# Optimization experiments

Measured on AMD Instinct MI355X. Metric: run time of the kernel, lower is better.

The kernel has to match this reference:

```python
import jax, jax.numpy as jnp
import numpy as np

B = 2048        # number of independent sample paths (batched simulation)
DIM = 64        # SDE state dimension
NSTEPS = 500    # Euler steps: (t1-t0)/dt0 = 1.0/0.002
DT0 = 0.002


def setup_inputs() -> dict:
    key = jax.random.key(0)
    ks = jax.random.split(key, 6)
    s = 0.5 / np.sqrt(DIM)  # keep the linear SDE stable over the horizon
    return {
        "x0": jax.random.normal(ks[0], (B, DIM), jnp.float32),
        # raw N(0,1) noise; scaled by sqrt(dt) inside reference (Brownian increments)
        "dW": jax.random.normal(ks[1], (B, NSTEPS, DIM), jnp.float32),
        "drift": jax.random.normal(ks[2], (DIM, DIM), jnp.float32) * s,
        "drift_bias": jax.random.normal(ks[3], (DIM,), jnp.float32) * 0.1,
        "diffusion": jax.random.normal(ks[4], (DIM, DIM), jnp.float32) * (0.1 * s),
        "diffusion_bias": jax.random.normal(ks[5], (DIM,), jnp.float32) * 0.1,
        "ts": jnp.arange(NSTEPS + 1, dtype=jnp.float32) * DT0,
    }


def reference(x0, dW, drift, drift_bias, diffusion, diffusion_bias, ts):
    """Euler-Maruyama for dx = (A x + b) dt + diag(C x + d) dW.

    Matches the diffrax Euler solver with SaveAt(ts) where ts lies on the
    fixed-step grid. diag(C x + d) @ dW == (C x + d) * dW elementwise.
    Returns ys: [B, NSTEPS+1, DIM] (saved states at every ts, incl. x0).
    """
    dts = jnp.diff(ts)                       # [NSTEPS]
    dW_t = jnp.swapaxes(dW, 0, 1)            # [NSTEPS, B, DIM]

    def step(x, inp):
        dt, dw = inp
        drift_v = x @ drift.T + drift_bias                 # [B, DIM]
        diff_v = x @ diffusion.T + diffusion_bias          # [B, DIM]
        x_next = x + dt * drift_v + diff_v * (jnp.sqrt(dt) * dw)
        return x_next, x_next

    _, ys = jax.lax.scan(step, x0, (dts, dW_t))            # [NSTEPS, B, DIM]
    ys = jnp.concatenate([x0[None], ys], axis=0)           # [NSTEPS+1, B, DIM]
    return jnp.swapaxes(ys, 0, 1)                          # [B, NSTEPS+1, DIM]
```

## Files before the change

### kernel.cpp

```cpp
#include <hip/hip_runtime.h>

#define NPATH  2048
#define DIM    64
#define NSTEPS 500
#define PPW    16

typedef __attribute__((ext_vector_type(8))) short bf16x8;
typedef __attribute__((ext_vector_type(4))) float f32x4;

union FragU { bf16x8 v; unsigned int u[4]; uint4 q; };

__device__ __forceinline__ unsigned int pk_bf16(float lo, float hi) {
    unsigned int r;
    asm("v_cvt_pk_bf16_f32 %0, %1, %2" : "=v"(r) : "v"(lo), "v"(hi));
    return r;
}

#define MFMA __builtin_amdgcn_mfma_f32_16x16x32_bf16

__global__ __launch_bounds__(256, 1) void sde_mfma_mw2_kernel(
    const float* __restrict__ x0,
    const float* __restrict__ dW,
    const float* __restrict__ drift,
    const float* __restrict__ drift_bias,
    const float* __restrict__ diffusion,
    const float* __restrict__ diffusion_bias,
    const float* __restrict__ ts,
    float* __restrict__ out)
{
    __shared__ __align__(16) unsigned short xt[2][PPW * DIM];
    __shared__ float2 dtp[NSTEPS + 1];

    const int tid   = threadIdx.x;
    const int wn    = tid >> 6;
    const int lane  = tid & 63;
    const int c     = lane & 15;
    const int h     = lane >> 4;
    const int pbase = blockIdx.x * PPW;
    const int mydim = 16 * wn + c;

    for (int i = tid; i < NSTEPS; i += 256) {
        const float d = ts[i + 1] - ts[i];
        dtp[i] = make_float2(d, sqrtf(d));
    }
    if (tid == 0) dtp[NSTEPS] = make_float2(0.f, 0.f);

    FragU bd0, bd1, bs0, bs1;
    {
        const float* Ar = drift     + mydim * DIM + 8 * h;
        const float* Cr = diffusion + mydim * DIM + 8 * h;
        float4 t;
        t = *(const float4*)(Ar +  0); bd0.u[0] = pk_bf16(t.x, t.y); bd0.u[1] = pk_bf16(t.z, t.w);
        t = *(const float4*)(Ar +  4); bd0.u[2] = pk_bf16(t.x, t.y); bd0.u[3] = pk_bf16(t.z, t.w);
        t = *(const float4*)(Ar + 32); bd1.u[0] = pk_bf16(t.x, t.y); bd1.u[1] = pk_bf16(t.z, t.w);
        t = *(const float4*)(Ar + 36); bd1.u[2] = pk_bf16(t.x, t.y); bd1.u[3] = pk_bf16(t.z, t.w);
        t = *(const float4*)(Cr +  0); bs0.u[0] = pk_bf16(t.x, t.y); bs0.u[1] = pk_bf16(t.z, t.w);
        t = *(const float4*)(Cr +  4); bs0.u[2] = pk_bf16(t.x, t.y); bs0.u[3] = pk_bf16(t.z, t.w);
        t = *(const float4*)(Cr + 32); bs1.u[0] = pk_bf16(t.x, t.y); bs1.u[1] = pk_bf16(t.z, t.w);
        t = *(const float4*)(Cr + 36); bs1.u[2] = pk_bf16(t.x, t.y); bs1.u[3] = pk_bf16(t.z, t.w);
    }
    const float bdr = drift_bias[mydim];
    const float bdi = diffusion_bias[mydim];
    const f32x4 cbA = {bdr, bdr, bdr, bdr};
    const f32x4 cbC = {bdi, bdi, bdi, bdi};
    const f32x4 cz  = {0.f, 0.f, 0.f, 0.f};

    float xst[4];
    const float* dwq[4];
    float* op[4];
    unsigned int woff[4];
#pragma unroll
    for (int j = 0; j < 4; ++j) {
        const int pp = 4 * h + j;
        const int p  = pbase + pp;
        dwq[j] = dW  + (size_t)p * NSTEPS * DIM + mydim;
        op[j]  = out + (size_t)p * (NSTEPS + 1) * DIM + mydim;
        woff[j] = (unsigned)((pp * 32 + ((mydim >> 1) ^ ((pp & 7) << 2))) * 2 + (c & 1));
        const float v = x0[p * DIM + mydim];
        xst[j] = v;
        __builtin_nontemporal_store(v, op[j]);
        op[j] += DIM;
        xt[0][woff[j]] = (unsigned short)pk_bf16(v, v);
    }

    const int ra0 = c * 8 + (h ^ (c & 7));
    const int ra1 = c * 8 + ((4 + h) ^ (c & 7));
    const uint4* xr0 = (const uint4*)xt[0];
    const uint4* xr1 = (const uint4*)xt[1];
    unsigned short* xw0 = xt[0];
    unsigned short* xw1 = xt[1];

    float R0[4], R1[4], R2[4], R3[4], R4[4], R5[4], R6[4], R7[4];
#pragma unroll
    for (int j = 0; j < 4; ++j) {
        R0[j] = dwq[j][0 * DIM]; R1[j] = dwq[j][1 * DIM];
        R2[j] = dwq[j][2 * DIM]; R3[j] = dwq[j][3 * DIM];
        R4[j] = dwq[j][4 * DIM]; R5[j] = dwq[j][5 * DIM];
        R6[j] = dwq[j][6 * DIM]; R7[j] = dwq[j][7 * DIM];
        dwq[j] += 8 * DIM;
    }

    __syncthreads();

    float2 dts = dtp[0];

#define STEP(S, R, PF, KOFF, XR, XW)                                          \
    {                                                                         \
        FragU a0, a1;                                                         \
        a0.q = XR[ra0];                                                       \
        a1.q = XR[ra1];                                                       \
        const float srw0 = dts.y * R[0];   \
        const float srw1 = dts.y * R[1];                                      \
        const float srw2 = dts.y * R[2];                                      \
        const float srw3 = dts.y * R[3];                                      \
        if (PF) {                                                             \
            R[0] = dwq[0][(KOFF) * DIM];                                      \
            R[1] = dwq[1][(KOFF) * DIM];                                      \
            R[2] = dwq[2][(KOFF) * DIM];                                      \
            R[3] = dwq[3][(KOFF) * DIM];                                      \
        }                                                                     \
        const float2 dtn = dtp[(S) + 1];                                      \
        const f32x4 adA = MFMA(a0.v, bd0.v, cbA, 0, 0, 0);                    \
        const f32x4 adB = MFMA(a1.v, bd1.v, cz,  0, 0, 0);                    \
        const f32x4 ciA = MFMA(a0.v, bs0.v, cbC, 0, 0, 0);                    \
        const f32x4 ciB = MFMA(a1.v, bs1.v, cz,  0, 0, 0);                    \
        const float srw[4] = {srw0, srw1, srw2, srw3};                        \
        _Pragma("unroll")                                                     \
        for (int j = 0; j < 4; ++j) {                                         \
            const float ad = adA[j] + adB[j];                                 \
            const float ci = ciA[j] + ciB[j];                                 \
            const float xn = fmaf(dts.x, ad, xst[j]) + ci * srw[j];           \
            xst[j] = xn;                                                      \
            __builtin_nontemporal_store(xn, op[j]);                           \
            op[j] += DIM;                                                     \
            XW[woff[j]] = (unsigned short)pk_bf16(xn, xn);                    \
        }                                                                     \
        dts = dtn;                                                            \
        asm volatile("s_waitcnt lgkmcnt(0)" ::: "memory");                    \
        __builtin_amdgcn_s_barrier();                                         \
        __builtin_amdgcn_sched_barrier(0);                                    \
    }

    for (int it = 0; it < 61; ++it) {
        const int s = it * 8;
        STEP(s + 0, R0, 1, 0, xr0, xw1)
        STEP(s + 1, R1, 1, 1, xr1, xw0)
        STEP(s + 2, R2, 1, 2, xr0, xw1)
        STEP(s + 3, R3, 1, 3, xr1, xw0)
        STEP(s + 4, R4, 1, 4, xr0, xw1)
        STEP(s + 5, R5, 1, 5, xr1, xw0)
        STEP(s + 6, R6, 1, 6, xr0, xw1)
        STEP(s + 7, R7, 1, 7, xr1, xw0)
#pragma unroll
        for (int j = 0; j < 4; ++j) dwq[j] += 8 * DIM;
    }
    {
        STEP(488, R0, 1, 0, xr0, xw1)
        STEP(489, R1, 1, 1, xr1, xw0)
        STEP(490, R2, 1, 2, xr0, xw1)
        STEP(491, R3, 1, 3, xr1, xw0)
        STEP(492, R4, 0, 0, xr0, xw1)
        STEP(493, R5, 0, 0, xr1, xw0)
        STEP(494, R6, 0, 0, xr0, xw1)
        STEP(495, R7, 0, 0, xr1, xw0)
    }
    {
        STEP(496, R0, 0, 0, xr0, xw1)
        STEP(497, R1, 0, 0, xr1, xw0)
        STEP(498, R2, 0, 0, xr0, xw1)
        STEP(499, R3, 0, 0, xr1, xw0)
    }
#undef STEP
}

extern "C" void kernel_launch(void* const* d_in, const int* in_sizes, int n_in,
                              void* d_out, int out_size, void* d_ws, size_t ws_size,
                              hipStream_t stream) {
    const float* x0             = (const float*)d_in[0];
    const float* dW             = (const float*)d_in[1];
    const float* drift          = (const float*)d_in[2];
    const float* drift_bias     = (const float*)d_in[3];
    const float* diffusion      = (const float*)d_in[4];
    const float* diffusion_bias = (const float*)d_in[5];
    const float* ts             = (const float*)d_in[6];
    float* out = (float*)d_out;

    dim3 grid(NPATH / PPW);
    dim3 block(256);
    hipLaunchKernelGGL(sde_mfma_mw2_kernel, grid, block, 0, stream,
                       x0, dW, drift, drift_bias, diffusion, diffusion_bias,
                       ts, out);
}
```

Before: 138.2 us.

## Stream dW noise through an 8-slot LDS ring via global_load_lds DMA

Replaces per-thread register prefetch of the Brownian increments with direct global-to-LDS 16-byte DMA loads into a per-wave 8-deep ring buffer, gated by vmcnt waits, and reads the noise back from LDS each step. This aims to cut VGPR pressure and the number of scalar global loads, and to keep loads in flight across several steps. It also changes the output stores from nontemporal to normal stores. The vmcnt(16) accounting now mixes DMA loads with output stores, which adds risk of too much or too little waiting, and each step pays extra LDS reads.

Measured after the change: 400.7 us. +189.9%, slower.

```diff
diff --git a/kernel.cpp b/kernel.cpp
--- a/kernel.cpp
+++ b/kernel.cpp
@@ -16,9 +16,15 @@
     return r;
 }
 
+__device__ __forceinline__ void dma16(const float* src, float* lds) {
+    __builtin_amdgcn_global_load_lds(
+        (const __attribute__((address_space(1))) void*)src,
+        (__attribute__((address_space(3))) void*)lds, 16, 0, 0);
+}
+
 #define MFMA __builtin_amdgcn_mfma_f32_16x16x32_bf16
 
-__global__ __launch_bounds__(256, 1) void sde_mfma_mw2_kernel(
+__global__ __launch_bounds__(256, 1) void sde_mfma_dma_kernel(
     const float* __restrict__ x0,
     const float* __restrict__ dW,
     const float* __restrict__ drift,
@@ -29,6 +35,7 @@
     float* __restrict__ out)
 {
     __shared__ __align__(16) unsigned short xt[2][PPW * DIM];
+    __shared__ __align__(16) float ring[4][8][256];
     __shared__ float2 dtp[NSTEPS + 1];
 
     const int tid   = threadIdx.x;
@@ -66,19 +73,17 @@
     const f32x4 cz  = {0.f, 0.f, 0.f, 0.f};
 
     float xst[4];
-    const float* dwq[4];
     float* op[4];
     unsigned int woff[4];
 #pragma unroll
     for (int j = 0; j < 4; ++j) {
         const int pp = 4 * h + j;
         const int p  = pbase + pp;
-        dwq[j] = dW  + (size_t)p * NSTEPS * DIM + mydim;
         op[j]  = out + (size_t)p * (NSTEPS + 1) * DIM + mydim;
         woff[j] = (unsigned)((pp * 32 + ((mydim >> 1) ^ ((pp & 7) << 2))) * 2 + (c & 1));
         const float v = x0[p * DIM + mydim];
         xst[j] = v;
-        __builtin_nontemporal_store(v, op[j]);
+        *op[j] = v;
         op[j] += DIM;
         xt[0][woff[j]] = (unsigned short)pk_bf16(v, v);
     }
@@ -90,41 +95,42 @@
     unsigned short* xw0 = xt[0];
     unsigned short* xw1 = xt[1];
 
-    float R0[4], R1[4], R2[4], R3[4], R4[4], R5[4], R6[4], R7[4];
+    const float* pdma = dW + (size_t)(pbase + (lane >> 2)) * NSTEPS * DIM
+                           + 16 * wn + 4 * (lane & 3);
+    float (*ringw)[256] = ring[wn];
+    const int rbase = h * 64 + c;
+
 #pragma unroll
-    for (int j = 0; j < 4; ++j) {
-        R0[j] = dwq[j][0 * DIM]; R1[j] = dwq[j][1 * DIM];
-        R2[j] = dwq[j][2 * DIM]; R3[j] = dwq[j][3 * DIM];
-        R4[j] = dwq[j][4 * DIM]; R5[j] = dwq[j][5 * DIM];
-        R6[j] = dwq[j][6 * DIM]; R7[j] = dwq[j][7 * DIM];
-        dwq[j] += 8 * DIM;
-    }
+    for (int s = 0; s < 7; ++s)
+        dma16(pdma + (size_t)s * DIM, &ringw[s][0]);
+    pdma += 7 * DIM;
 
+    asm volatile("s_waitcnt vmcnt(0)" ::: "memory");
+    __builtin_amdgcn_sched_barrier(0);
     __syncthreads();
 
     float2 dts = dtp[0];
+    const float2* pdt = &dtp[1];
 
-#define STEP(S, R, PF, KOFF, XR, XW)                                          \
+#define STEP(K, DODMA, XR, XW)                                                \
     {                                                                         \
+        asm volatile("s_waitcnt vmcnt(16)" ::: "memory");                     \
+        __builtin_amdgcn_sched_barrier(0);                                    \
         FragU a0, a1;                                                         \
         a0.q = XR[ra0];                                                       \
         a1.q = XR[ra1];                                                       \
-        const float srw0 = dts.y * R[0];   \
-        const float srw1 = dts.y * R[1];                                      \
-        const float srw2 = dts.y * R[2];                                      \
-        const float srw3 = dts.y * R[3];                                      \
-        if (PF) {                                                             \
-            R[0] = dwq[0][(KOFF) * DIM];                                      \
-            R[1] = dwq[1][(KOFF) * DIM];                                      \
-            R[2] = dwq[2][(KOFF) * DIM];                                      \
-            R[3] = dwq[3][(KOFF) * DIM];                                      \
-        }                                                                     \
-        const float2 dtn = dtp[(S) + 1];                                      \
+        const float r0 = ringw[K][rbase +  0];                                \
+        const float r1 = ringw[K][rbase + 16];                                \
+        const float r2 = ringw[K][rbase + 32];                                \
+        const float r3 = ringw[K][rbase + 48];                                \
+        if (DODMA) dma16(pdma, &ringw[(K + 7) & 7][0]);                       \
+        pdma += DIM;                                                          \
+        const float2 dtn = *pdt++;                                            \
         const f32x4 adA = MFMA(a0.v, bd0.v, cbA, 0, 0, 0);                    \
         const f32x4 adB = MFMA(a1.v, bd1.v, cz,  0, 0, 0);                    \
         const f32x4 ciA = MFMA(a0.v, bs0.v, cbC, 0, 0, 0);                    \
         const f32x4 ciB = MFMA(a1.v, bs1.v, cz,  0, 0, 0);                    \
-        const float srw[4] = {srw0, srw1, srw2, srw3};                        \
+        const float srw[4] = {dts.y * r0, dts.y * r1, dts.y * r2, dts.y * r3};\
         _Pragma("unroll")                                                     \
         for (int j = 0; j < 4; ++j) {                                         \
             const float ad = adA[j] + adB[j];                                 \
@@ -142,34 +148,27 @@
     }
 
     for (int it = 0; it < 61; ++it) {
-        const int s = it * 8;
-        STEP(s + 0, R0, 1, 0, xr0, xw1)
-        STEP(s + 1, R1, 1, 1, xr1, xw0)
-        STEP(s + 2, R2, 1, 2, xr0, xw1)
-        STEP(s + 3, R3, 1, 3, xr1, xw0)
-        STEP(s + 4, R4, 1, 4, xr0, xw1)
-        STEP(s + 5, R5, 1, 5, xr1, xw0)
-        STEP(s + 6, R6, 1, 6, xr0, xw1)
-        STEP(s + 7, R7, 1, 7, xr1, xw0)
-#pragma unroll
-        for (int j = 0; j < 4; ++j) dwq[j] += 8 * DIM;
+        STEP(0, 1, xr0, xw1)
+        STEP(1, 1, xr1, xw0)
+        STEP(2, 1, xr0, xw1)
+        STEP(3, 1, xr1, xw0)
+        STEP(4, 1, xr0, xw1)
+        STEP(5, 1, xr1, xw0)
+        STEP(6, 1, xr0, xw1)
+        STEP(7, 1, xr1, xw0)
     }
-    {
-        STEP(488, R0, 1, 0, xr0, xw1)
-        STEP(489, R1, 1, 1, xr1, xw0)
-        STEP(490, R2, 1, 2, xr0, xw1)
-        STEP(491, R3, 1, 3, xr1, xw0)
-        STEP(492, R4, 0, 0, xr0, xw1)
-        STEP(493, R5, 0, 0, xr1, xw0)
-        STEP(494, R6, 0, 0, xr0, xw1)
-        STEP(495, R7, 0, 0, xr1, xw0)
-    }
-    {
-        STEP(496, R0, 0, 0, xr0, xw1)
-        STEP(497, R1, 0, 0, xr1, xw0)
-        STEP(498, R2, 0, 0, xr0, xw1)
-        STEP(499, R3, 0, 0, xr1, xw0)
-    }
+    STEP(0, 1, xr0, xw1)
+    STEP(1, 1, xr1, xw0)
+    STEP(2, 1, xr0, xw1)
+    STEP(3, 1, xr1, xw0)
+    STEP(4, 1, xr0, xw1)
+    STEP(5, 0, xr1, xw0)
+    STEP(6, 0, xr0, xw1)
+    STEP(7, 0, xr1, xw0)
+    STEP(0, 0, xr0, xw1)
+    STEP(1, 0, xr1, xw0)
+    STEP(2, 0, xr0, xw1)
+    STEP(3, 0, xr1, xw0)
 #undef STEP
 }
 
@@ -187,7 +186,7 @@
 
     dim3 grid(NPATH / PPW);
     dim3 block(256);
-    hipLaunchKernelGGL(sde_mfma_mw2_kernel, grid, block, 0, stream,
+    hipLaunchKernelGGL(sde_mfma_dma_kernel, grid, block, 0, stream,
                        x0, dW, drift, drift_bias, diffusion, diffusion_bias,
                        ts, out);
 }
```
